# Kernel optimization log

Hardware: AMD Instinct MI355X
Metric: run time of the kernel (lower is better)

## Reference

```python
import jax, jax.numpy as jnp
import numpy as np

B, T, D, H = 4, 2048, 1024, 16
DK = D // H

def setup_inputs() -> dict:
    key = jax.random.key(0)
    k1, k2, k3 = jax.random.split(key, 3)
    s = 1.0 / np.sqrt(D)
    return {
        "x": jax.random.normal(k1, (B, T, D), dtype=jnp.float32),
        "W_qkv": jax.random.normal(k2, (D, 3 * D), dtype=jnp.float32) * s,
        "b_qkv": jnp.zeros((3 * D,), dtype=jnp.float32),
        "W_out": jax.random.normal(k3, (D, D), dtype=jnp.float32) * s,
        "b_out": jnp.zeros((D,), dtype=jnp.float32),
    }

def reference(x, W_qkv, b_qkv, W_out, b_out):
    Bx, Tx, C = x.shape
    qkv = x @ W_qkv + b_qkv                       # [B,T,3D]
    q, k, v = jnp.split(qkv, 3, axis=-1)
    # [B,T,D] -> [B,H,T,dk]
    def heads(t):
        return t.reshape(Bx, Tx, H, DK).transpose(0, 2, 1, 3)
    q, k, v = heads(q), heads(k), heads(v)
    scores = jnp.einsum('bhqd,bhkd->bhqk', q, k) / jnp.sqrt(jnp.float32(DK))
    causal = jnp.tril(jnp.ones((Tx, Tx), dtype=bool))  # [T,T]
    scores = jnp.where(causal[None, None], scores, -jnp.inf)
    attn = jax.nn.softmax(scores, axis=-1)        # dropout p=0 (eval)
    out = jnp.einsum('bhqk,bhkd->bhqd', attn, v)  # [B,H,T,dk]
    out = out.transpose(0, 2, 1, 3).reshape(Bx, Tx, C)
    return out @ W_out + b_out
```

## Files before the change

### kernel.cpp

```cpp
#include <hip/hip_runtime.h>
#include <hip/hip_bf16.h>
#include <stdint.h>

#define T_SEQ 2048
#define DMODEL 1024
#define NH 16
#define DKH 64
#define M_TOK 8192
#define N_QKV 3072
#define K_DIM 1024

#define ATTN_SC (0.125f * 1.44269504f)

typedef __attribute__((ext_vector_type(8))) short short8;
typedef __attribute__((ext_vector_type(4))) short short4v;
typedef __attribute__((ext_vector_type(4))) float float4v;
typedef __attribute__((ext_vector_type(2))) unsigned int uint2v;

__device__ inline short bf16_bits(float f) {
  __hip_bfloat16 h = __float2bfloat16(f);
  short s;
  __builtin_memcpy(&s, &h, 2);
  return s;
}

__device__ inline short4v pack4_bf16_fast(float a, float b, float c, float d) {
  unsigned ua = __builtin_bit_cast(unsigned, a) + 0x8000u;
  unsigned ub = __builtin_bit_cast(unsigned, b) + 0x8000u;
  unsigned uc = __builtin_bit_cast(unsigned, c) + 0x8000u;
  unsigned ud = __builtin_bit_cast(unsigned, d) + 0x8000u;
  uint2v uu = {(ua >> 16) | (ub & 0xFFFF0000u),
               (uc >> 16) | (ud & 0xFFFF0000u)};
  return __builtin_bit_cast(short4v, uu);
}

__device__ inline short4v pack4_bf16_trunc(float a, float b, float c, float d) {
  unsigned ua = __builtin_bit_cast(unsigned, a);
  unsigned ub = __builtin_bit_cast(unsigned, b);
  unsigned uc = __builtin_bit_cast(unsigned, c);
  unsigned ud = __builtin_bit_cast(unsigned, d);
  uint2v uu = {__builtin_amdgcn_perm(ub, ua, 0x07060302u),
               __builtin_amdgcn_perm(ud, uc, 0x07060302u)};
  return __builtin_bit_cast(short4v, uu);
}

__device__ inline void async_load16(const void* g, void* l) {
  __builtin_amdgcn_global_load_lds(
      (const __attribute__((address_space(1))) unsigned int*)g,
      (__attribute__((address_space(3))) unsigned int*)l,
      16, 0, 0);
}


__global__ __launch_bounds__(256) void cvt_kernel(const float* __restrict__ in,
                                                  short* __restrict__ out, int n) {
  int idx = (blockIdx.x * 256 + threadIdx.x) * 4;
  if (idx < n) {
    float4v v = *(const float4v*)(in + idx);
    short4v o;
    o[0] = bf16_bits(v[0]); o[1] = bf16_bits(v[1]);
    o[2] = bf16_bits(v[2]); o[3] = bf16_bits(v[3]);
    *(short4v*)(out + idx) = o;
  }
}

__global__ __launch_bounds__(256) void transpose_cvt(const float* __restrict__ in,
                                                     short* __restrict__ out,
                                                     int K, int N) {
  __shared__ float tile[32][33];
  int n0 = blockIdx.x * 32, k0 = blockIdx.y * 32;
  int tx = threadIdx.x, ty = threadIdx.y;
  #pragma unroll
  for (int r = ty; r < 32; r += 8)
    tile[r][tx] = in[(size_t)(k0 + r) * N + n0 + tx];
  __syncthreads();
  #pragma unroll
  for (int r = ty; r < 32; r += 8)
    out[(size_t)(n0 + r) * K + k0 + tx] = bf16_bits(tile[tx][r]);
}


template <int EPI>
__global__ __launch_bounds__(256) void gemm_bt(
    const short* __restrict__ A, const short* __restrict__ Bt,
    const float* __restrict__ bias,
    short* __restrict__ Qb, short* __restrict__ Kf, short* __restrict__ Vf,
    float* __restrict__ Cout, int M, int N, int K, int ntile0) {
  constexpr bool CT = (EPI != 1);
  __shared__ __align__(16) short AsB[2][128 * 32];
  __shared__ __align__(16) short BsB[2][128 * 32];
  const int tid = threadIdx.x;
  const int lane = tid & 63;
  const int wave = tid >> 6;
  const int m0 = blockIdx.x * 128;
  const int n0 = (blockIdx.y + ntile0) * 128;
  const int wm = (wave >> 1) * 64;
  const int wn = (wave & 1) * 64;
  const int quad = lane >> 4;
  const int l16 = lane & 15;

  float4v acc[4][4] = {};

  const int r0 = tid >> 2, r1 = r0 + 64;
  const int oswz = (((tid & 3) - (tid >> 3)) & 3) * 8;
  const int lo0 = wave * 512;
  const int lo1 = 2048 + wave * 512;

  const short* Ag0 = A  + (size_t)(m0 + r0) * K + oswz;
  const short* Ag1 = A  + (size_t)(m0 + r1) * K + oswz;
  const short* Bg0 = Bt + (size_t)(n0 + r0) * K + oswz;
  const short* Bg1 = Bt + (size_t)(n0 + r1) * K + oswz;

  const int sw = ((quad + (l16 >> 1)) & 3) * 8;

  async_load16(Ag0, &AsB[0][0] + lo0);
  async_load16(Ag1, &AsB[0][0] + lo1);
  async_load16(Bg0, &BsB[0][0] + lo0);
  async_load16(Bg1, &BsB[0][0] + lo1);

  const int nkt = K >> 5;
  for (int it = 0; it < nkt; ++it) {
    __builtin_amdgcn_s_waitcnt(0);
    __syncthreads();

    if (it + 1 < nkt) {
      const int kt = (it + 1) << 5;
      const int nb = (it + 1) & 1;
      async_load16(Ag0 + kt, &AsB[nb][0] + lo0);
      async_load16(Ag1 + kt, &AsB[nb][0] + lo1);
      async_load16(Bg0 + kt, &BsB[nb][0] + lo0);
      async_load16(Bg1 + kt, &BsB[nb][0] + lo1);
    }

    const short* As = &AsB[it & 1][0];
    const short* Bs = &BsB[it & 1][0];
    short8 af[4], bfr[4];
    #pragma unroll
    for (int t = 0; t < 4; ++t)
      af[t] = *(const short8*)(As + (size_t)(wm + t * 16 + l16) * 32 + sw);
    #pragma unroll
    for (int t = 0; t < 4; ++t)
      bfr[t] = *(const short8*)(Bs + (size_t)(wn + t * 16 + l16) * 32 + sw);
    #pragma unroll
    for (int i = 0; i < 4; ++i)
      #pragma unroll
      for (int j = 0; j < 4; ++j) {
        if (CT)
          acc[i][j] = __builtin_amdgcn_mfma_f32_16x16x32_bf16(bfr[j], af[i], acc[i][j], 0, 0, 0);
        else
          acc[i][j] = __builtin_amdgcn_mfma_f32_16x16x32_bf16(af[i], bfr[j], acc[i][j], 0, 0, 0);
      }
  }

  if (EPI == 0) {
    const int which = n0 >> 10;
    #pragma unroll
    for (int tj = 0; tj < 4; ++tj) {
      const int colb = n0 + wn + tj * 16 + quad * 4;
      float4v bz = *(const float4v*)(bias + colb);
      const int d = colb & 1023;
      const int h = d >> 6, dkb = d & 63;
      #pragma unroll
      for (int ti = 0; ti < 4; ++ti) {
        const int tok = m0 + wm + ti * 16 + l16;
        const int b = tok >> 11, t = tok & 2047;
        const size_t bhoff = (size_t)(b * NH + h) * (T_SEQ * DKH);
        float4v v = acc[ti][tj];
        if (which == 0) {
          short4v o = pack4_bf16_fast((v[0] + bz[0]) * ATTN_SC, (v[1] + bz[1]) * ATTN_SC,
                                      (v[2] + bz[2]) * ATTN_SC, (v[3] + bz[3]) * ATTN_SC);
          *(short4v*)(Qb + bhoff + (size_t)t * DKH + dkb) = o;
        } else {
          short4v o = pack4_bf16_fast(v[0] + bz[0], v[1] + bz[1], v[2] + bz[2], v[3] + bz[3]);
          const int h2 = dkb >> 5, qd = (dkb >> 3) & 3, w = dkb & 7;
          size_t kbase = bhoff + (size_t)(t >> 6) * 4096 +
                         ((((t >> 4) & 3) * 2 + h2) * 4 + qd) * 128 + (t & 15) * 8 + w;
          *(short4v*)(Kf + kbase) = o;
        }
      }
    }
  } else if (EPI == 1) {
    #pragma unroll
    for (int tj = 0; tj < 4; ++tj) {
      const int col = n0 + wn + tj * 16 + l16;
      const float bz = bias[col];
      const int d = col & 1023;
      const int h = d >> 6, dk = d & 63;
      #pragma unroll
      for (int ti = 0; ti < 4; ++ti) {
        const int rbase = m0 + wm + ti * 16 + quad * 4;
        const int b = rbase >> 11, t = rbase & 2047;
        const size_t bhoff = (size_t)(b * NH + h) * (T_SEQ * DKH);
        float4v v = acc[ti][tj];
        short4v pv = pack4_bf16_fast(v[0] + bz, v[1] + bz, v[2] + bz, v[3] + bz);
        size_t off = bhoff + (size_t)(t >> 6) * 4096 +
                     ((((t >> 4) & 3) * 4 + (dk >> 4)) * 4 + ((t >> 2) & 3)) * 64 +
                     (dk & 15) * 4;
        *(short4v*)(Vf + off) = pv;
      }
    }
  } else {
    #pragma unroll
    for (int tj = 0; tj < 4; ++tj) {
      const int colb = n0 + wn + tj * 16 + quad * 4;
      float4v bz = *(const float4v*)(bias + colb);
      #pragma unroll
      for (int ti = 0; ti < 4; ++ti) {
        const int row = m0 + wm + ti * 16 + l16;
        float4v v = acc[ti][tj];
        float4v o = {v[0] + bz[0], v[1] + bz[1], v[2] + bz[2], v[3] + bz[3]};
        *(float4v*)(Cout + (size_t)row * N + colb) = o;
      }
    }
  }
}


template <int MASK>
__device__ __forceinline__ void attn_tile(
    const short* __restrict__ Ks, const short* __restrict__ Vs,
    const short8 aq[2][2], short4v ones,
    float4v oc[2][4], float4v lc[2],
    int dkq, int quad, int l16) {
  const int mb = dkq + quad * 4 - l16;
  #pragma unroll
  for (int c = 0; c < 4; ++c) {
    short8 b0 = *(const short8*)(Ks + (c * 2 + 0) * 512 + quad * 128 + l16 * 8);
    short8 b1 = *(const short8*)(Ks + (c * 2 + 1) * 512 + quad * 128 + l16 * 8);
    short4v vf[4];
    #pragma unroll
    for (int d = 0; d < 4; ++d)
      vf[d] = *(const short4v*)(Vs + (c * 4 + d) * 256 + quad * 64 + l16 * 4);
    #pragma unroll
    for (int qi = 0; qi < 2; ++qi) {
      float4v z = {0.f, 0.f, 0.f, 0.f};
      z = __builtin_amdgcn_mfma_f32_16x16x32_bf16(b0, aq[qi][0], z, 0, 0, 0);
      z = __builtin_amdgcn_mfma_f32_16x16x32_bf16(b1, aq[qi][1], z, 0, 0, 0);
      float p[4];
      #pragma unroll
      for (int i = 0; i < 4; ++i) {
        p[i] = __builtin_amdgcn_exp2f(z[i]);
        if (MASK && (mb + c * 16 + i - qi * 16 > 0)) p[i] = 0.f;
      }
      short4v pb = pack4_bf16_trunc(p[0], p[1], p[2], p[3]);
      lc[qi] = __builtin_amdgcn_mfma_f32_16x16x16bf16_1k(ones, pb, lc[qi], 0, 0, 0);
      #pragma unroll
      for (int d = 0; d < 4; ++d)
        oc[qi][d] = __builtin_amdgcn_mfma_f32_16x16x16bf16_1k(vf[d], pb, oc[qi][d], 0, 0, 0);
    }
  }
}

__global__ __launch_bounds__(256) void attn_kernel(const short* __restrict__ Qb,
                                                   const short* __restrict__ Kf,
                                                   const short* __restrict__ Vf,
                                                   short* __restrict__ Ao) {
  __shared__ __align__(16) short KsB[2][4096];
  __shared__ __align__(16) short VsB[2][4096];
  const int bh = blockIdx.x;
  const int y = blockIdx.y;
  const int qb = (y < 4) ? (15 - y) : (y < 8) ? (y - 4) : (y < 12) ? (19 - y) : (y - 8);
  const int tid = threadIdx.x;
  const int lane = tid & 63, wave = tid >> 6;
  const int quad = lane >> 4, l16 = lane & 15;
  const int qw0 = qb * 128 + wave * 32;
  const int nkb = 2 * qb + 2;

  const short* Qg = Qb + ((size_t)bh * T_SEQ + qw0) * DKH;
  const short* Kg0 = Kf + (size_t)bh * (T_SEQ * DKH);
  const short* Vg0 = Vf + (size_t)bh * (T_SEQ * DKH);

  short8 aq[2][2];
  #pragma unroll
  for (int qi = 0; qi < 2; ++qi)
    #pragma unroll
    for (int h = 0; h < 2; ++h)
      aq[qi][h] = *(const short8*)(Qg + (size_t)(qi * 16 + l16) * DKH + h * 32 + quad * 8);

  float4v oc[2][4] = {};
  float4v lc[2] = {};
  short4v ones = {0x3F80, 0x3F80, 0x3F80, 0x3F80};

  async_load16(Kg0 + tid * 8,        &KsB[0][0] + wave * 512);
  async_load16(Kg0 + 2048 + tid * 8, &KsB[0][0] + 2048 + wave * 512);
  async_load16(Vg0 + tid * 8,        &VsB[0][0] + wave * 512);
  async_load16(Vg0 + 2048 + tid * 8, &VsB[0][0] + 2048 + wave * 512);

  for (int kb = 0; kb < nkb; ++kb) {
    __builtin_amdgcn_s_waitcnt(0);
    __syncthreads();

    if (kb + 1 < nkb) {
      const int nb = (kb + 1) & 1;
      const short* Kg = Kg0 + (size_t)(kb + 1) * 4096;
      const short* Vg = Vg0 + (size_t)(kb + 1) * 4096;
      async_load16(Kg + tid * 8,        &KsB[nb][0] + wave * 512);
      async_load16(Kg + 2048 + tid * 8, &KsB[nb][0] + 2048 + wave * 512);
      async_load16(Vg + tid * 8,        &VsB[nb][0] + wave * 512);
      async_load16(Vg + 2048 + tid * 8, &VsB[nb][0] + 2048 + wave * 512);
    }

    const int dkq = kb * 64 - qw0;
    if (dkq + 63 <= 0) {
      attn_tile<0>(&KsB[kb & 1][0], &VsB[kb & 1][0], aq, ones, oc, lc, dkq, quad, l16);
    } else if (dkq <= 31) {
      attn_tile<1>(&KsB[kb & 1][0], &VsB[kb & 1][0], aq, ones, oc, lc, dkq, quad, l16);
    }
  }

  const int b = bh >> 4, h = bh & 15;
  #pragma unroll
  for (int qi = 0; qi < 2; ++qi) {
    float rl = 1.0f / lc[qi][0];
    #pragma unroll
    for (int d = 0; d < 4; ++d) {
      float4v v = oc[qi][d];
      short4v o = pack4_bf16_fast(v[0] * rl, v[1] * rl, v[2] * rl, v[3] * rl);
      int t = qw0 + qi * 16 + l16;
      *(short4v*)(Ao + (size_t)(b * T_SEQ + t) * DMODEL + h * DKH + d * 16 + quad * 4) = o;
    }
  }
}


extern "C" void kernel_launch(void* const* d_in, const int* in_sizes, int n_in,
                              void* d_out, int out_size, void* d_ws, size_t ws_size,
                              hipStream_t stream) {
  const float* x    = (const float*)d_in[0];
  const float* Wqkv = (const float*)d_in[1];
  const float* bqkv = (const float*)d_in[2];
  const float* Wout = (const float*)d_in[3];
  const float* bout = (const float*)d_in[4];
  float* out = (float*)d_out;

  char* ws = (char*)d_ws;
  short* Xb    = (short*)(ws);
  short* Wqkvt = (short*)(ws + (16ull << 20));
  short* Woutt = (short*)(ws + (22ull << 20));
  short* Qb    = (short*)(ws + (24ull << 20));
  short* Kf    = (short*)(ws + (40ull << 20));
  short* Vf    = (short*)(ws + (56ull << 20));
  short* Ao    = (short*)(ws + (72ull << 20));

  cvt_kernel<<<(M_TOK * K_DIM / 4 + 255) / 256, 256, 0, stream>>>(x, Xb, M_TOK * K_DIM);
  dim3 tb(32, 8);
  transpose_cvt<<<dim3(N_QKV / 32, K_DIM / 32), tb, 0, stream>>>(Wqkv, Wqkvt, K_DIM, N_QKV);
  transpose_cvt<<<dim3(DMODEL / 32, K_DIM / 32), tb, 0, stream>>>(Wout, Woutt, K_DIM, DMODEL);

  gemm_bt<0><<<dim3(M_TOK / 128, 16), 256, 0, stream>>>(
      Xb, Wqkvt, bqkv, Qb, Kf, nullptr, nullptr, M_TOK, N_QKV, K_DIM, 0);
  gemm_bt<1><<<dim3(M_TOK / 128, 8), 256, 0, stream>>>(
      Xb, Wqkvt, bqkv, nullptr, nullptr, Vf, nullptr, M_TOK, N_QKV, K_DIM, 16);

  attn_kernel<<<dim3(64, T_SEQ / 128), 256, 0, stream>>>(Qb, Kf, Vf, Ao);

  gemm_bt<2><<<dim3(M_TOK / 128, DMODEL / 128), 256, 0, stream>>>(
      Ao, Woutt, bout, nullptr, nullptr, nullptr, out, M_TOK, DMODEL, K_DIM, 0);
}
```

Baseline: 248.2 us.

## Read K/V tiles directly from global memory per wave, dropping LDS double-buffering

The attention kernel no longer stages K and V blocks into shared memory with async copies, double buffering and a block-wide barrier. Each wave now loops over only the key blocks its own 32 queries need, calling the tile routine with global pointers, and applies the causal mask on the last block only. This removes the per-iteration barriers and the fully masked iterations some waves used to sit through. In exchange, all four waves fetch the same K/V data separately through the cache hierarchy, and global-load latency is no longer hidden behind prefetching.

```diff
diff --git a/kernel.cpp b/kernel.cpp
--- a/kernel.cpp
+++ b/kernel.cpp
@@ -255,8 +255,6 @@
                                                    const short* __restrict__ Kf,
                                                    const short* __restrict__ Vf,
                                                    short* __restrict__ Ao) {
-  __shared__ __align__(16) short KsB[2][4096];
-  __shared__ __align__(16) short VsB[2][4096];
   const int bh = blockIdx.x;
   const int y = blockIdx.y;
   const int qb = (y < 4) ? (15 - y) : (y < 8) ? (y - 4) : (y < 12) ? (19 - y) : (y - 8);
@@ -264,7 +262,6 @@
   const int lane = tid & 63, wave = tid >> 6;
   const int quad = lane >> 4, l16 = lane & 15;
   const int qw0 = qb * 128 + wave * 32;
-  const int nkb = 2 * qb + 2;
 
   const short* Qg = Qb + ((size_t)bh * T_SEQ + qw0) * DKH;
   const short* Kg0 = Kf + (size_t)bh * (T_SEQ * DKH);
@@ -281,31 +278,14 @@
   float4v lc[2] = {};
   short4v ones = {0x3F80, 0x3F80, 0x3F80, 0x3F80};
 
-  async_load16(Kg0 + tid * 8,        &KsB[0][0] + wave * 512);
-  async_load16(Kg0 + 2048 + tid * 8, &KsB[0][0] + 2048 + wave * 512);
-  async_load16(Vg0 + tid * 8,        &VsB[0][0] + wave * 512);
-  async_load16(Vg0 + 2048 + tid * 8, &VsB[0][0] + 2048 + wave * 512);
-
-  for (int kb = 0; kb < nkb; ++kb) {
-    __builtin_amdgcn_s_waitcnt(0);
-    __syncthreads();
-
-    if (kb + 1 < nkb) {
-      const int nb = (kb + 1) & 1;
-      const short* Kg = Kg0 + (size_t)(kb + 1) * 4096;
-      const short* Vg = Vg0 + (size_t)(kb + 1) * 4096;
-      async_load16(Kg + tid * 8,        &KsB[nb][0] + wave * 512);
-      async_load16(Kg + 2048 + tid * 8, &KsB[nb][0] + 2048 + wave * 512);
-      async_load16(Vg + tid * 8,        &VsB[nb][0] + wave * 512);
-      async_load16(Vg + 2048 + tid * 8, &VsB[nb][0] + 2048 + wave * 512);
-    }
-
-    const int dkq = kb * 64 - qw0;
-    if (dkq + 63 <= 0) {
-      attn_tile<0>(&KsB[kb & 1][0], &VsB[kb & 1][0], aq, ones, oc, lc, dkq, quad, l16);
-    } else if (dkq <= 31) {
-      attn_tile<1>(&KsB[kb & 1][0], &VsB[kb & 1][0], aq, ones, oc, lc, dkq, quad, l16);
-    }
+  const int nkbw = (qw0 + 95) >> 6;
+  for (int kb = 0; kb < nkbw - 1; ++kb)
+    attn_tile<0>(Kg0 + (size_t)kb * 4096, Vg0 + (size_t)kb * 4096,
+                 aq, ones, oc, lc, 0, quad, l16);
+  {
+    const int kb = nkbw - 1;
+    attn_tile<1>(Kg0 + (size_t)kb * 4096, Vg0 + (size_t)kb * 4096,
+                 aq, ones, oc, lc, kb * 64 - qw0, quad, l16);
   }
 
   const int b = bh >> 4, h = bh & 15;
```

Measured after the change: 269.4 us. 8.6% more time.
